# Performance work log

Measured on AMD Instinct MI355X. Metric: run time of the kernel, lower is better.

The kernel has to match this reference:

```python
import jax, jax.numpy as jnp
import numpy as np

E, H, F, T, K = 32, 1024, 512, 1024, 8

def setup_inputs() -> dict:
    key = jax.random.key(0)
    k1, k2, k3, k4, k5 = jax.random.split(key, 5)
    return {
        "hidden_states": jax.random.normal(k1, (T, H), dtype=jnp.float32),
        "top_k_index": jax.random.randint(k2, (T, K), 0, E),
        "top_k_weights": jax.random.uniform(k3, (T, K), dtype=jnp.float32),
        "gate_up_proj": jax.random.normal(k4, (E, 2 * F, H), dtype=jnp.float32),
        "down_proj": jax.random.normal(k5, (E, H, F), dtype=jnp.float32),
    }

def reference(hidden_states, top_k_index, top_k_weights, gate_up_proj, down_proj):
    n_experts = gate_up_proj.shape[0]
    T_ = hidden_states.shape[0]
    # Combine routing weights into dense [T, E] map (duplicates accumulate,
    # matching torch's index_add_ semantics).
    w = jnp.zeros((T_, n_experts), dtype=hidden_states.dtype)
    w = w.at[jnp.arange(T_)[:, None], top_k_index].add(top_k_weights)
    ffn = down_proj.shape[-1]

    def step(final, params):
        Wgu, Wd, we = params  # [2F,H], [H,F], [T]
        gu = hidden_states @ Wgu.T            # [T, 2F]
        gate, up = gu[:, :ffn], gu[:, ffn:]
        out = (jax.nn.silu(gate) * up) @ Wd.T  # [T, H]
        return final + we[:, None] * out, None

    final, _ = jax.lax.scan(step, jnp.zeros_like(hidden_states),
                            (gate_up_proj, down_proj, w.T))
    return final
```

## Files before the change

### kernel.cpp

```cpp
#include <hip/hip_runtime.h>
#include <hip/hip_bf16.h>

#define NE     32
#define HD     1024
#define FF     512
#define NT     1024
#define TOPK   8
#define NPAIR  (NT * TOPK)
#define MAXT2  96

typedef __attribute__((ext_vector_type(8))) short  bf16x8;
typedef __attribute__((ext_vector_type(4))) float  f32x4;

__device__ __forceinline__ unsigned short f2bf_rne(float f) {
    unsigned u = __float_as_uint(f);
    u += 0x7FFFu + ((u >> 16) & 1u);
    return (unsigned short)(u >> 16);
}
__device__ __forceinline__ unsigned pk2(float x, float y) {
    __hip_bfloat162 h = __float22bfloat162_rn(float2{x, y});
    union { __hip_bfloat162 h; unsigned u; } c;
    c.h = h;
    return c.u;
}
__device__ __forceinline__ uint4 pk8q(float4 a, float4 b) {
    uint4 r;
    r.x = pk2(a.x, a.y); r.y = pk2(a.z, a.w);
    r.z = pk2(b.x, b.y); r.w = pk2(b.z, b.w);
    return r;
}
__device__ __forceinline__ bf16x8 pk8r(float4 a, float4 b) {
    union { unsigned u[4]; bf16x8 v; } r;
    r.u[0] = pk2(a.x, a.y); r.u[1] = pk2(a.z, a.w);
    r.u[2] = pk2(b.x, b.y); r.u[3] = pk2(b.z, b.w);
    return r.v;
}
__device__ __forceinline__ void gload16(const void* g, void* l) {
    __builtin_amdgcn_global_load_lds(
        (const __attribute__((address_space(1))) unsigned int*)g,
        (__attribute__((address_space(3))) unsigned int*)l, 16, 0, 0);
}
#define MFMA16(a, b, c) __builtin_amdgcn_mfma_f32_16x16x32_bf16(a, b, c, 0, 0, 0)

#define PIPE_SYNC() do {                                   \
    asm volatile("s_waitcnt vmcnt(6)" ::: "memory");       \
    __builtin_amdgcn_s_barrier();                          \
    __builtin_amdgcn_sched_barrier(0);                     \
} while (0)

#define OFF_XG (128u * 1024u)
#define OFF_AB (OFF_XG + 8320u * 2048u)
#define OFF_O  (OFF_AB + 8320u * 1024u)

__global__ __launch_bounds__(1024) void k_route(const int* __restrict__ idx,
                                                const float* __restrict__ tkw,
                                                int* __restrict__ meta) {
    __shared__ int sc[NE], scur[NE], soff[NE + 1];
    __shared__ int ste[MAXT2], stm[MAXT2], snt;
    int tid = threadIdx.x;
    if (tid < NE) { sc[tid] = 0; scur[tid] = 0; }
    __syncthreads();
    int e8[TOPK];
#pragma unroll
    for (int j = 0; j < TOPK; j++) { e8[j] = idx[tid * TOPK + j]; atomicAdd(&sc[e8[j]], 1); }
    __syncthreads();
    if (tid == 0) {
        int off = 0, nt = 0;
        for (int e = 0; e < NE; e++) {
            soff[e] = off;
            for (int s = 0; s < sc[e]; s += 128) { ste[nt] = e; stm[nt] = s; nt++; }
            off += sc[e];
        }
        soff[NE] = off; snt = nt;
    }
    __syncthreads();
    int*   tok_list = meta + 256;
    float* w_list   = (float*)(meta + 8448);
    int*   posmap   = meta + 16640;
#pragma unroll
    for (int j = 0; j < TOPK; j++) {
        int e = e8[j];
        int p = soff[e] + atomicAdd(&scur[e], 1);
        tok_list[p] = tid;
        w_list[p]   = tkw[tid * TOPK + j];
        posmap[tid * TOPK + j] = p;
    }
    if (tid <= NE) meta[1 + tid] = soff[tid];
    if (tid == 0)  meta[0] = snt;
    if (tid < MAXT2) { meta[64 + tid] = (tid < snt) ? ste[tid] : 0;
                       meta[160 + tid] = (tid < snt) ? stm[tid] : 0; }
}

__global__ void k_gather(const float* __restrict__ hs, const int* __restrict__ meta,
                         unsigned short* __restrict__ Xg) {
    int i = blockIdx.x * blockDim.x + threadIdx.x;
    int p = i >> 7, c = (i & 127) << 3;
    int tok = meta[256 + p];
    float4 a = *(const float4*)(hs + (size_t)tok * HD + c);
    float4 b = *(const float4*)(hs + (size_t)tok * HD + c + 4);
    *(uint4*)(Xg + (size_t)p * HD + c) = pk8q(a, b);
}

__global__ __launch_bounds__(256, 2) void k_mm1(
        const unsigned short* __restrict__ Xg, const float* __restrict__ wgu,
        const int* __restrict__ meta, const float* __restrict__ w_list,
        unsigned short* __restrict__ A) {
    int lid = blockIdx.x;
    int wsw = (lid & 7) * 96 + (lid >> 3);
    int bx = wsw >> 3, by = wsw & 7;
    int numt = meta[0];
    if (bx >= numt) return;
    int e   = meta[64 + bx], m0 = meta[160 + bx];
    int seg = meta[1 + e];
    int nrows = meta[2 + e] - seg - m0;
    if (nrows > 128) nrows = 128;
    int c0 = by * 64;

    __shared__ __align__(16) unsigned char Xb0[8192];
    __shared__ __align__(16) unsigned char Xb1[8192];
    __shared__ __align__(16) unsigned char Xb2[8192];
    int tid = threadIdx.x;
    int wave = tid >> 6, lane = tid & 63, lr = lane & 15, lk = lane >> 4;

    unsigned Lp0 = (unsigned)(wave * 2) * 1024u + (unsigned)lane * 16u;
    unsigned Lp1 = Lp0 + 1024u;
    unsigned ldsoff0 = Lp0, ldsoff1 = Lp1;
    const unsigned char* xsrc0 = (const unsigned char*)Xg +
        (size_t)(seg + m0 + (Lp0 >> 6)) * (HD * 2) + ((Lp0 & 63u) ^ (((Lp0 >> 7) & 3u) << 4));
    const unsigned char* xsrc1 = (const unsigned char*)Xg +
        (size_t)(seg + m0 + (Lp1 >> 6)) * (HD * 2) + ((Lp1 & 63u) ^ (((Lp1 >> 7) & 3u) << 4));

    int cp = c0 + wave * 16 + lr;
    const float* gp = wgu + ((size_t)e * 2 * FF + cp) * HD + lk * 8;
    const float* up = gp + (size_t)FF * HD;

    unsigned aoff[8];
#pragma unroll
    for (int mf = 0; mf < 8; mf++) {
        unsigned row = mf * 16 + lr;
        aoff[mf] = row * 64 + (((unsigned)lk * 16) ^ (((row >> 1) & 3u) << 4));
    }

    f32x4 acc[8][2] = {};
    float4 wsA[4], wsB[4];
    const unsigned char* cur = Xb0;
    const unsigned char* nxt = Xb1;
    const unsigned char* fut = Xb2;

    gload16(xsrc0, Xb0 + ldsoff0); gload16(xsrc1, Xb0 + ldsoff1);
    xsrc0 += 64; xsrc1 += 64;
    gload16(xsrc0, Xb1 + ldsoff0); gload16(xsrc1, Xb1 + ldsoff1);
    xsrc0 += 64; xsrc1 += 64;
    wsA[0] = *(const float4*)(gp);     wsA[1] = *(const float4*)(gp + 4);
    wsA[2] = *(const float4*)(up);     wsA[3] = *(const float4*)(up + 4);
    int wk = 32;

    auto step = [&](float4 (&wuse)[4], float4 (&wld)[4], bool doX, bool doW) {
        PIPE_SYNC();
        if (doX) {
            gload16(xsrc0, (void*)(fut + ldsoff0));
            gload16(xsrc1, (void*)(fut + ldsoff1));
            xsrc0 += 64; xsrc1 += 64;
        }
        if (doW) {
            wld[0] = *(const float4*)(gp + wk);     wld[1] = *(const float4*)(gp + wk + 4);
            wld[2] = *(const float4*)(up + wk);     wld[3] = *(const float4*)(up + wk + 4);
            wk += 32;
        }
        bf16x8 bg = pk8r(wuse[0], wuse[1]);
        bf16x8 bu = pk8r(wuse[2], wuse[3]);
#pragma unroll
        for (int mf = 0; mf < 8; mf++) {
            bf16x8 af = *(const bf16x8*)(cur + aoff[mf]);
            acc[mf][0] = MFMA16(af, bg, acc[mf][0]);
            acc[mf][1] = MFMA16(af, bu, acc[mf][1]);
        }
        const unsigned char* t = cur; cur = nxt; nxt = fut; fut = t;
    };

    for (int t2 = 0; t2 < 14; t2++) {
        step(wsA, wsB, true, true);
        step(wsB, wsA, true, true);
    }
    step(wsA, wsB, true,  true);
    step(wsB, wsA, true,  true);
    step(wsA, wsB, false, true);
    step(wsB, wsA, false, false);

#pragma unroll
    for (int mf = 0; mf < 8; mf++)
#pragma unroll
        for (int q = 0; q < 4; q++) {
            int r = mf * 16 + lk * 4 + q;
            if (r < nrows) {
                float w = w_list[seg + m0 + r];
                float g = acc[mf][0][q], u = acc[mf][1][q];
                float act = (g / (1.f + __expf(-g))) * u * w;
                A[(size_t)(seg + m0 + r) * FF + cp] = f2bf_rne(act);
            }
        }
}

__global__ __launch_bounds__(256, 2) void k_mm2(
        const unsigned short* __restrict__ A, const float* __restrict__ wd,
        const int* __restrict__ meta, float* __restrict__ O) {
    int lid = blockIdx.x;
    int wsw = (lid & 7) * 96 + (lid >> 3);
    int bx = wsw >> 3, by = wsw & 7;
    int numt = meta[0];
    if (bx >= numt) return;
    int e   = meta[64 + bx], m0 = meta[160 + bx];
    int seg = meta[1 + e];
    int nrows = meta[2 + e] - seg - m0;
    if (nrows > 128) nrows = 128;
    int n0 = by * 128;

    __shared__ __align__(16) unsigned char Xb0[8192];
    __shared__ __align__(16) unsigned char Xb1[8192];
    __shared__ __align__(16) unsigned char Xb2[8192];
    int tid = threadIdx.x;
    int wave = tid >> 6, lane = tid & 63, lr = lane & 15, lk = lane >> 4;

    unsigned Lp0 = (unsigned)(wave * 2) * 1024u + (unsigned)lane * 16u;
    unsigned Lp1 = Lp0 + 1024u;
    unsigned ldsoff0 = Lp0, ldsoff1 = Lp1;
    const unsigned char* xsrc0 = (const unsigned char*)A +
        (size_t)(seg + m0 + (Lp0 >> 6)) * (FF * 2) + ((Lp0 & 63u) ^ (((Lp0 >> 7) & 3u) << 4));
    const unsigned char* xsrc1 = (const unsigned char*)A +
        (size_t)(seg + m0 + (Lp1 >> 6)) * (FF * 2) + ((Lp1 & 63u) ^ (((Lp1 >> 7) & 3u) << 4));

    int n_a = n0 + wave * 32 + lr;
    int n_b = n_a + 16;
    const float* wpa = wd + ((size_t)e * HD + n_a) * FF + lk * 8;
    const float* wpb = wd + ((size_t)e * HD + n_b) * FF + lk * 8;

    unsigned aoff[8];
#pragma unroll
    for (int mf = 0; mf < 8; mf++) {
        unsigned row = mf * 16 + lr;
        aoff[mf] = row * 64 + (((unsigned)lk * 16) ^ (((row >> 1) & 3u) << 4));
    }

    f32x4 acc[8][2] = {};
    float4 wsA[4], wsB[4];
    const unsigned char* cur = Xb0;
    const unsigned char* nxt = Xb1;
    const unsigned char* fut = Xb2;

    gload16(xsrc0, Xb0 + ldsoff0); gload16(xsrc1, Xb0 + ldsoff1);
    xsrc0 += 64; xsrc1 += 64;
    gload16(xsrc0, Xb1 + ldsoff0); gload16(xsrc1, Xb1 + ldsoff1);
    xsrc0 += 64; xsrc1 += 64;
    wsA[0] = *(const float4*)(wpa);    wsA[1] = *(const float4*)(wpa + 4);
    wsA[2] = *(const float4*)(wpb);    wsA[3] = *(const float4*)(wpb + 4);
    int wk = 32;

    auto step = [&](float4 (&wuse)[4], float4 (&wld)[4], bool doX, bool doW) {
        PIPE_SYNC();
        if (doX) {
            gload16(xsrc0, (void*)(fut + ldsoff0));
            gload16(xsrc1, (void*)(fut + ldsoff1));
            xsrc0 += 64; xsrc1 += 64;
        }
        if (doW) {
            wld[0] = *(const float4*)(wpa + wk);   wld[1] = *(const float4*)(wpa + wk + 4);
            wld[2] = *(const float4*)(wpb + wk);   wld[3] = *(const float4*)(wpb + wk + 4);
            wk += 32;
        }
        bf16x8 b0 = pk8r(wuse[0], wuse[1]);
        bf16x8 b1 = pk8r(wuse[2], wuse[3]);
#pragma unroll
        for (int mf = 0; mf < 8; mf++) {
            bf16x8 af = *(const bf16x8*)(cur + aoff[mf]);
            acc[mf][0] = MFMA16(af, b0, acc[mf][0]);
            acc[mf][1] = MFMA16(af, b1, acc[mf][1]);
        }
        const unsigned char* t = cur; cur = nxt; nxt = fut; fut = t;
    };

    for (int t2 = 0; t2 < 6; t2++) {
        step(wsA, wsB, true, true);
        step(wsB, wsA, true, true);
    }
    step(wsA, wsB, true,  true);
    step(wsB, wsA, true,  true);
    step(wsA, wsB, false, true);
    step(wsB, wsA, false, false);

#pragma unroll
    for (int mf = 0; mf < 8; mf++)
#pragma unroll
        for (int q = 0; q < 4; q++) {
            int r = mf * 16 + lk * 4 + q;
            if (r < nrows) {
                O[(size_t)(seg + m0 + r) * HD + n_a] = acc[mf][0][q];
                O[(size_t)(seg + m0 + r) * HD + n_b] = acc[mf][1][q];
            }
        }
}

__global__ void k_reduce(const float* __restrict__ O, const int* __restrict__ posmap,
                         float* __restrict__ out) {
    int i = blockIdx.x * blockDim.x + threadIdx.x;
    int t = i >> 8, c4 = i & 255;
    float4 acc = make_float4(0.f, 0.f, 0.f, 0.f);
#pragma unroll
    for (int k = 0; k < TOPK; k++) {
        int p = posmap[t * TOPK + k];
        float4 v = ((const float4*)(O + (size_t)p * HD))[c4];
        acc.x += v.x; acc.y += v.y; acc.z += v.z; acc.w += v.w;
    }
    ((float4*)out)[i] = acc;
}

extern "C" void kernel_launch(void* const* d_in, const int* in_sizes, int n_in,
                              void* d_out, int out_size, void* d_ws, size_t ws_size,
                              hipStream_t stream) {
    const float* hs  = (const float*)d_in[0];
    const int*   idx = (const int*)  d_in[1];
    const float* tkw = (const float*)d_in[2];
    const float* wgu = (const float*)d_in[3];
    const float* wd  = (const float*)d_in[4];
    float* out = (float*)d_out;

    char* ws = (char*)d_ws;
    int* meta = (int*)ws;
    unsigned short* Xg   = (unsigned short*)(ws + OFF_XG);
    unsigned short* A_bf = (unsigned short*)(ws + OFF_AB);
    float* O_rows        = (float*)(ws + OFF_O);
    const float* w_list  = (const float*)(meta + 8448);
    const int* posmap    = meta + 16640;

    k_route<<<1, 1024, 0, stream>>>(idx, tkw, meta);
    k_gather<<<NPAIR * (HD / 8) / 256, 256, 0, stream>>>(hs, meta, Xg);
    k_mm1<<<MAXT2 * 8, 256, 0, stream>>>(Xg, wgu, meta, w_list, A_bf);
    k_mm2<<<MAXT2 * 8, 256, 0, stream>>>(A_bf, wd, meta, O_rows);
    k_reduce<<<NT * HD / 4 / 256, 256, 0, stream>>>(O_rows, posmap, out);
}
```

Measured before the change: 140.6 us.

## Split GEMM tiles across 8 waves and deepen weight-prefetch pipeline

Both expert GEMM kernels now launch 512 threads (8 waves) per block instead of 256. The 128-row tile is split into two 64-row halves across wave pairs, so each wave holds half the accumulators. Each thread issues a single LDS async load per stage. The register weight prefetch gains a third buffer, so global weight loads are issued two steps ahead, with the vmcnt wait adjusted and a full drain on the last step. The aim is more waves in flight to hide global latency and lower register pressure, at the cost of loading each weight fragment twice (once per row-half wave).

```diff
diff --git a/kernel.cpp b/kernel.cpp
--- a/kernel.cpp
+++ b/kernel.cpp
@@ -42,10 +42,11 @@
 }
 #define MFMA16(a, b, c) __builtin_amdgcn_mfma_f32_16x16x32_bf16(a, b, c, 0, 0, 0)
 
-#define PIPE_SYNC() do {                                   \
-    asm volatile("s_waitcnt vmcnt(6)" ::: "memory");       \
-    __builtin_amdgcn_s_barrier();                          \
-    __builtin_amdgcn_sched_barrier(0);                     \
+#define PIPE_SYNC(LAST) do {                                       \
+    if (LAST) asm volatile("s_waitcnt vmcnt(0)" ::: "memory");     \
+    else      asm volatile("s_waitcnt vmcnt(5)" ::: "memory");     \
+    __builtin_amdgcn_s_barrier();                                  \
+    __builtin_amdgcn_sched_barrier(0);                             \
 } while (0)
 
 #define OFF_XG (128u * 1024u)
@@ -101,7 +102,7 @@
     *(uint4*)(Xg + (size_t)p * HD + c) = pk8q(a, b);
 }
 
-__global__ __launch_bounds__(256, 2) void k_mm1(
+__global__ __launch_bounds__(512, 4) void k_mm1(
         const unsigned short* __restrict__ Xg, const float* __restrict__ wgu,
         const int* __restrict__ meta, const float* __restrict__ w_list,
         unsigned short* __restrict__ A) {
@@ -121,48 +122,43 @@
     __shared__ __align__(16) unsigned char Xb2[8192];
     int tid = threadIdx.x;
     int wave = tid >> 6, lane = tid & 63, lr = lane & 15, lk = lane >> 4;
-
-    unsigned Lp0 = (unsigned)(wave * 2) * 1024u + (unsigned)lane * 16u;
-    unsigned Lp1 = Lp0 + 1024u;
-    unsigned ldsoff0 = Lp0, ldsoff1 = Lp1;
-    const unsigned char* xsrc0 = (const unsigned char*)Xg +
-        (size_t)(seg + m0 + (Lp0 >> 6)) * (HD * 2) + ((Lp0 & 63u) ^ (((Lp0 >> 7) & 3u) << 4));
-    const unsigned char* xsrc1 = (const unsigned char*)Xg +
-        (size_t)(seg + m0 + (Lp1 >> 6)) * (HD * 2) + ((Lp1 & 63u) ^ (((Lp1 >> 7) & 3u) << 4));
-
-    int cp = c0 + wave * 16 + lr;
+    int wave_m = wave >> 2, wave_n = wave & 3;
+
+    unsigned Lp = (unsigned)wave * 1024u + (unsigned)lane * 16u;
+    unsigned ldsoff = Lp;
+    const unsigned char* xsrc = (const unsigned char*)Xg +
+        (size_t)(seg + m0 + (Lp >> 6)) * (HD * 2) + ((Lp & 63u) ^ (((Lp >> 7) & 3u) << 4));
+
+    int cp = c0 + wave_n * 16 + lr;
     const float* gp = wgu + ((size_t)e * 2 * FF + cp) * HD + lk * 8;
     const float* up = gp + (size_t)FF * HD;
 
-    unsigned aoff[8];
-#pragma unroll
-    for (int mf = 0; mf < 8; mf++) {
-        unsigned row = mf * 16 + lr;
+    unsigned aoff[4];
+#pragma unroll
+    for (int mf = 0; mf < 4; mf++) {
+        unsigned row = wave_m * 64 + mf * 16 + lr;
         aoff[mf] = row * 64 + (((unsigned)lk * 16) ^ (((row >> 1) & 3u) << 4));
     }
 
-    f32x4 acc[8][2] = {};
-    float4 wsA[4], wsB[4];
+    f32x4 acc[4][2] = {};
+    float4 wsA[4], wsB[4], wsC[4];
     const unsigned char* cur = Xb0;
     const unsigned char* nxt = Xb1;
     const unsigned char* fut = Xb2;
 
-    gload16(xsrc0, Xb0 + ldsoff0); gload16(xsrc1, Xb0 + ldsoff1);
-    xsrc0 += 64; xsrc1 += 64;
-    gload16(xsrc0, Xb1 + ldsoff0); gload16(xsrc1, Xb1 + ldsoff1);
-    xsrc0 += 64; xsrc1 += 64;
-    wsA[0] = *(const float4*)(gp);     wsA[1] = *(const float4*)(gp + 4);
-    wsA[2] = *(const float4*)(up);     wsA[3] = *(const float4*)(up + 4);
-    int wk = 32;
-
-    auto step = [&](float4 (&wuse)[4], float4 (&wld)[4], bool doX, bool doW) {
-        PIPE_SYNC();
-        if (doX) {
-            gload16(xsrc0, (void*)(fut + ldsoff0));
-            gload16(xsrc1, (void*)(fut + ldsoff1));
-            xsrc0 += 64; xsrc1 += 64;
-        }
-        if (doW) {
+    gload16(xsrc, Xb0 + ldsoff); xsrc += 64;
+    gload16(xsrc, Xb1 + ldsoff); xsrc += 64;
+    __builtin_amdgcn_sched_barrier(0);
+    wsA[0] = *(const float4*)(gp);      wsA[1] = *(const float4*)(gp + 4);
+    wsA[2] = *(const float4*)(up);      wsA[3] = *(const float4*)(up + 4);
+    wsB[0] = *(const float4*)(gp + 32); wsB[1] = *(const float4*)(gp + 36);
+    wsB[2] = *(const float4*)(up + 32); wsB[3] = *(const float4*)(up + 36);
+    int wk = 64;
+
+    auto step = [&](float4 (&wuse)[4], float4 (&wld)[4], bool iss, bool last) {
+        PIPE_SYNC(last);
+        if (iss) {
+            gload16(xsrc, (void*)(fut + ldsoff)); xsrc += 64;
             wld[0] = *(const float4*)(gp + wk);     wld[1] = *(const float4*)(gp + wk + 4);
             wld[2] = *(const float4*)(up + wk);     wld[3] = *(const float4*)(up + wk + 4);
             wk += 32;
@@ -170,7 +166,7 @@
         bf16x8 bg = pk8r(wuse[0], wuse[1]);
         bf16x8 bu = pk8r(wuse[2], wuse[3]);
 #pragma unroll
-        for (int mf = 0; mf < 8; mf++) {
+        for (int mf = 0; mf < 4; mf++) {
             bf16x8 af = *(const bf16x8*)(cur + aoff[mf]);
             acc[mf][0] = MFMA16(af, bg, acc[mf][0]);
             acc[mf][1] = MFMA16(af, bu, acc[mf][1]);
@@ -178,20 +174,19 @@
         const unsigned char* t = cur; cur = nxt; nxt = fut; fut = t;
     };
 
-    for (int t2 = 0; t2 < 14; t2++) {
-        step(wsA, wsB, true, true);
-        step(wsB, wsA, true, true);
-    }
-    step(wsA, wsB, true,  true);
-    step(wsB, wsA, true,  true);
-    step(wsA, wsB, false, true);
-    step(wsB, wsA, false, false);
-
-#pragma unroll
-    for (int mf = 0; mf < 8; mf++)
+    for (int i = 0; i < 10; i++) {
+        step(wsA, wsC, true, false);
+        step(wsB, wsA, true, false);
+        step(wsC, wsB, true, false);
+    }
+    step(wsA, wsC, false, false);
+    step(wsB, wsA, false, true);
+
+#pragma unroll
+    for (int mf = 0; mf < 4; mf++)
 #pragma unroll
         for (int q = 0; q < 4; q++) {
-            int r = mf * 16 + lk * 4 + q;
+            int r = wave_m * 64 + mf * 16 + lk * 4 + q;
             if (r < nrows) {
                 float w = w_list[seg + m0 + r];
                 float g = acc[mf][0][q], u = acc[mf][1][q];
@@ -201,7 +196,7 @@
         }
 }
 
-__global__ __launch_bounds__(256, 2) void k_mm2(
+__global__ __launch_bounds__(512, 4) void k_mm2(
         const unsigned short* __restrict__ A, const float* __restrict__ wd,
         const int* __restrict__ meta, float* __restrict__ O) {
     int lid = blockIdx.x;
@@ -220,49 +215,44 @@
     __shared__ __align__(16) unsigned char Xb2[8192];
     int tid = threadIdx.x;
     int wave = tid >> 6, lane = tid & 63, lr = lane & 15, lk = lane >> 4;
-
-    unsigned Lp0 = (unsigned)(wave * 2) * 1024u + (unsigned)lane * 16u;
-    unsigned Lp1 = Lp0 + 1024u;
-    unsigned ldsoff0 = Lp0, ldsoff1 = Lp1;
-    const unsigned char* xsrc0 = (const unsigned char*)A +
-        (size_t)(seg + m0 + (Lp0 >> 6)) * (FF * 2) + ((Lp0 & 63u) ^ (((Lp0 >> 7) & 3u) << 4));
-    const unsigned char* xsrc1 = (const unsigned char*)A +
-        (size_t)(seg + m0 + (Lp1 >> 6)) * (FF * 2) + ((Lp1 & 63u) ^ (((Lp1 >> 7) & 3u) << 4));
-
-    int n_a = n0 + wave * 32 + lr;
+    int wave_m = wave >> 2, wave_n = wave & 3;
+
+    unsigned Lp = (unsigned)wave * 1024u + (unsigned)lane * 16u;
+    unsigned ldsoff = Lp;
+    const unsigned char* xsrc = (const unsigned char*)A +
+        (size_t)(seg + m0 + (Lp >> 6)) * (FF * 2) + ((Lp & 63u) ^ (((Lp >> 7) & 3u) << 4));
+
+    int n_a = n0 + wave_n * 32 + lr;
     int n_b = n_a + 16;
     const float* wpa = wd + ((size_t)e * HD + n_a) * FF + lk * 8;
     const float* wpb = wd + ((size_t)e * HD + n_b) * FF + lk * 8;
 
-    unsigned aoff[8];
-#pragma unroll
-    for (int mf = 0; mf < 8; mf++) {
-        unsigned row = mf * 16 + lr;
+    unsigned aoff[4];
+#pragma unroll
+    for (int mf = 0; mf < 4; mf++) {
+        unsigned row = wave_m * 64 + mf * 16 + lr;
         aoff[mf] = row * 64 + (((unsigned)lk * 16) ^ (((row >> 1) & 3u) << 4));
     }
 
-    f32x4 acc[8][2] = {};
-    float4 wsA[4], wsB[4];
+    f32x4 acc[4][2] = {};
+    float4 wsA[4], wsB[4], wsC[4];
     const unsigned char* cur = Xb0;
     const unsigned char* nxt = Xb1;
     const unsigned char* fut = Xb2;
 
-    gload16(xsrc0, Xb0 + ldsoff0); gload16(xsrc1, Xb0 + ldsoff1);
-    xsrc0 += 64; xsrc1 += 64;
-    gload16(xsrc0, Xb1 + ldsoff0); gload16(xsrc1, Xb1 + ldsoff1);
-    xsrc0 += 64; xsrc1 += 64;
-    wsA[0] = *(const float4*)(wpa);    wsA[1] = *(const float4*)(wpa + 4);
-    wsA[2] = *(const float4*)(wpb);    wsA[3] = *(const float4*)(wpb + 4);
-    int wk = 32;
-
-    auto step = [&](float4 (&wuse)[4], float4 (&wld)[4], bool doX, bool doW) {
-        PIPE_SYNC();
-        if (doX) {
-            gload16(xsrc0, (void*)(fut + ldsoff0));
-            gload16(xsrc1, (void*)(fut + ldsoff1));
-            xsrc0 += 64; xsrc1 += 64;
-        }
-        if (doW) {
+    gload16(xsrc, Xb0 + ldsoff); xsrc += 64;
+    gload16(xsrc, Xb1 + ldsoff); xsrc += 64;
+    __builtin_amdgcn_sched_barrier(0);
+    wsA[0] = *(const float4*)(wpa);      wsA[1] = *(const float4*)(wpa + 4);
+    wsA[2] = *(const float4*)(wpb);      wsA[3] = *(const float4*)(wpb + 4);
+    wsB[0] = *(const float4*)(wpa + 32); wsB[1] = *(const float4*)(wpa + 36);
+    wsB[2] = *(const float4*)(wpb + 32); wsB[3] = *(const float4*)(wpb + 36);
+    int wk = 64;
+
+    auto step = [&](float4 (&wuse)[4], float4 (&wld)[4], bool iss, bool last) {
+        PIPE_SYNC(last);
+        if (iss) {
+            gload16(xsrc, (void*)(fut + ldsoff)); xsrc += 64;
             wld[0] = *(const float4*)(wpa + wk);   wld[1] = *(const float4*)(wpa + wk + 4);
             wld[2] = *(const float4*)(wpb + wk);   wld[3] = *(const float4*)(wpb + wk + 4);
             wk += 32;
@@ -270,7 +260,7 @@
         bf16x8 b0 = pk8r(wuse[0], wuse[1]);
         bf16x8 b1 = pk8r(wuse[2], wuse[3]);
 #pragma unroll
-        for (int mf = 0; mf < 8; mf++) {
+        for (int mf = 0; mf < 4; mf++) {
             bf16x8 af = *(const bf16x8*)(cur + aoff[mf]);
             acc[mf][0] = MFMA16(af, b0, acc[mf][0]);
             acc[mf][1] = MFMA16(af, b1, acc[mf][1]);
@@ -278,20 +268,21 @@
         const unsigned char* t = cur; cur = nxt; nxt = fut; fut = t;
     };
 
-    for (int t2 = 0; t2 < 6; t2++) {
-        step(wsA, wsB, true, true);
-        step(wsB, wsA, true, true);
-    }
-    step(wsA, wsB, true,  true);
-    step(wsB, wsA, true,  true);
-    step(wsA, wsB, false, true);
-    step(wsB, wsA, false, false);
-
-#pragma unroll
-    for (int mf = 0; mf < 8; mf++)
+    for (int i = 0; i < 4; i++) {
+        step(wsA, wsC, true, false);
+        step(wsB, wsA, true, false);
+        step(wsC, wsB, true, false);
+    }
+    step(wsA, wsC, true,  false);
+    step(wsB, wsA, true,  false);
+    step(wsC, wsB, false, false);
+    step(wsA, wsC, false, true);
+
+#pragma unroll
+    for (int mf = 0; mf < 4; mf++)
 #pragma unroll
         for (int q = 0; q < 4; q++) {
-            int r = mf * 16 + lk * 4 + q;
+            int r = wave_m * 64 + mf * 16 + lk * 4 + q;
             if (r < nrows) {
                 O[(size_t)(seg + m0 + r) * HD + n_a] = acc[mf][0][q];
                 O[(size_t)(seg + m0 + r) * HD + n_b] = acc[mf][1][q];
@@ -333,7 +324,7 @@
 
     k_route<<<1, 1024, 0, stream>>>(idx, tkw, meta);
     k_gather<<<NPAIR * (HD / 8) / 256, 256, 0, stream>>>(hs, meta, Xg);
-    k_mm1<<<MAXT2 * 8, 256, 0, stream>>>(Xg, wgu, meta, w_list, A_bf);
-    k_mm2<<<MAXT2 * 8, 256, 0, stream>>>(A_bf, wd, meta, O_rows);
+    k_mm1<<<MAXT2 * 8, 512, 0, stream>>>(Xg, wgu, meta, w_list, A_bf);
+    k_mm2<<<MAXT2 * 8, 512, 0, stream>>>(A_bf, wd, meta, O_rows);
     k_reduce<<<NT * HD / 4 / 256, 256, 0, stream>>>(O_rows, posmap, out);
 }
```

Measured after the change: 197.9 us. 1.41x slower.

## Split MoE GEMM tiles into 2x2 wave layout with half-width N tiles

Applied to the files above, without the earlier changes.

Both grouped GEMM kernels now use a narrower N tile (32 columns for mm1, 64 for mm2) and arrange the four waves as a 2x2 grid over M and N instead of four waves across N. This doubles the number of blocks to fill more CUs, halves per-wave accumulators so occupancy can rise to 4 blocks per CU, and adds a full vmcnt(0) wait before the last step. The cost is that each X tile in LDS is reloaded by twice as many blocks, and each weight column is read by two waves.

```diff
diff --git a/kernel.cpp b/kernel.cpp
--- a/kernel.cpp
+++ b/kernel.cpp
@@ -42,10 +42,11 @@
 }
 #define MFMA16(a, b, c) __builtin_amdgcn_mfma_f32_16x16x32_bf16(a, b, c, 0, 0, 0)
 
-#define PIPE_SYNC() do {                                   \
-    asm volatile("s_waitcnt vmcnt(6)" ::: "memory");       \
-    __builtin_amdgcn_s_barrier();                          \
-    __builtin_amdgcn_sched_barrier(0);                     \
+#define PIPE_SYNC(LAST) do {                                       \
+    if (LAST) asm volatile("s_waitcnt vmcnt(0)" ::: "memory");     \
+    else      asm volatile("s_waitcnt vmcnt(6)" ::: "memory");     \
+    __builtin_amdgcn_s_barrier();                                  \
+    __builtin_amdgcn_sched_barrier(0);                             \
 } while (0)
 
 #define OFF_XG (128u * 1024u)
@@ -101,26 +102,27 @@
     *(uint4*)(Xg + (size_t)p * HD + c) = pk8q(a, b);
 }
 
-__global__ __launch_bounds__(256, 2) void k_mm1(
+__global__ __launch_bounds__(256, 4) void k_mm1(
         const unsigned short* __restrict__ Xg, const float* __restrict__ wgu,
         const int* __restrict__ meta, const float* __restrict__ w_list,
         unsigned short* __restrict__ A) {
     int lid = blockIdx.x;
-    int wsw = (lid & 7) * 96 + (lid >> 3);
-    int bx = wsw >> 3, by = wsw & 7;
+    int wsw = (lid & 7) * 192 + (lid >> 3);
+    int bx = wsw >> 4, by = wsw & 15;
     int numt = meta[0];
     if (bx >= numt) return;
     int e   = meta[64 + bx], m0 = meta[160 + bx];
     int seg = meta[1 + e];
     int nrows = meta[2 + e] - seg - m0;
     if (nrows > 128) nrows = 128;
-    int c0 = by * 64;
+    int c0 = by * 32;
 
     __shared__ __align__(16) unsigned char Xb0[8192];
     __shared__ __align__(16) unsigned char Xb1[8192];
     __shared__ __align__(16) unsigned char Xb2[8192];
     int tid = threadIdx.x;
     int wave = tid >> 6, lane = tid & 63, lr = lane & 15, lk = lane >> 4;
+    int wave_m = wave >> 1, wave_n = wave & 1;
 
     unsigned Lp0 = (unsigned)(wave * 2) * 1024u + (unsigned)lane * 16u;
     unsigned Lp1 = Lp0 + 1024u;
@@ -130,18 +132,18 @@
     const unsigned char* xsrc1 = (const unsigned char*)Xg +
         (size_t)(seg + m0 + (Lp1 >> 6)) * (HD * 2) + ((Lp1 & 63u) ^ (((Lp1 >> 7) & 3u) << 4));
 
-    int cp = c0 + wave * 16 + lr;
+    int cp = c0 + wave_n * 16 + lr;
     const float* gp = wgu + ((size_t)e * 2 * FF + cp) * HD + lk * 8;
     const float* up = gp + (size_t)FF * HD;
 
-    unsigned aoff[8];
-#pragma unroll
-    for (int mf = 0; mf < 8; mf++) {
-        unsigned row = mf * 16 + lr;
+    unsigned aoff[4];
+#pragma unroll
+    for (int mf = 0; mf < 4; mf++) {
+        unsigned row = wave_m * 64 + mf * 16 + lr;
         aoff[mf] = row * 64 + (((unsigned)lk * 16) ^ (((row >> 1) & 3u) << 4));
     }
 
-    f32x4 acc[8][2] = {};
+    f32x4 acc[4][2] = {};
     float4 wsA[4], wsB[4];
     const unsigned char* cur = Xb0;
     const unsigned char* nxt = Xb1;
@@ -155,8 +157,8 @@
     wsA[2] = *(const float4*)(up);     wsA[3] = *(const float4*)(up + 4);
     int wk = 32;
 
-    auto step = [&](float4 (&wuse)[4], float4 (&wld)[4], bool doX, bool doW) {
-        PIPE_SYNC();
+    auto step = [&](float4 (&wuse)[4], float4 (&wld)[4], bool doX, bool doW, bool last) {
+        PIPE_SYNC(last);
         if (doX) {
             gload16(xsrc0, (void*)(fut + ldsoff0));
             gload16(xsrc1, (void*)(fut + ldsoff1));
@@ -170,7 +172,7 @@
         bf16x8 bg = pk8r(wuse[0], wuse[1]);
         bf16x8 bu = pk8r(wuse[2], wuse[3]);
 #pragma unroll
-        for (int mf = 0; mf < 8; mf++) {
+        for (int mf = 0; mf < 4; mf++) {
             bf16x8 af = *(const bf16x8*)(cur + aoff[mf]);
             acc[mf][0] = MFMA16(af, bg, acc[mf][0]);
             acc[mf][1] = MFMA16(af, bu, acc[mf][1]);
@@ -179,19 +181,19 @@
     };
 
     for (int t2 = 0; t2 < 14; t2++) {
-        step(wsA, wsB, true, true);
-        step(wsB, wsA, true, true);
-    }
-    step(wsA, wsB, true,  true);
-    step(wsB, wsA, true,  true);
-    step(wsA, wsB, false, true);
-    step(wsB, wsA, false, false);
-
-#pragma unroll
-    for (int mf = 0; mf < 8; mf++)
+        step(wsA, wsB, true, true, false);
+        step(wsB, wsA, true, true, false);
+    }
+    step(wsA, wsB, true,  true,  false);
+    step(wsB, wsA, true,  true,  false);
+    step(wsA, wsB, false, true,  false);
+    step(wsB, wsA, false, false, true);
+
+#pragma unroll
+    for (int mf = 0; mf < 4; mf++)
 #pragma unroll
         for (int q = 0; q < 4; q++) {
-            int r = mf * 16 + lk * 4 + q;
+            int r = wave_m * 64 + mf * 16 + lk * 4 + q;
             if (r < nrows) {
                 float w = w_list[seg + m0 + r];
                 float g = acc[mf][0][q], u = acc[mf][1][q];
@@ -201,25 +203,26 @@
         }
 }
 
-__global__ __launch_bounds__(256, 2) void k_mm2(
+__global__ __launch_bounds__(256, 4) void k_mm2(
         const unsigned short* __restrict__ A, const float* __restrict__ wd,
         const int* __restrict__ meta, float* __restrict__ O) {
     int lid = blockIdx.x;
-    int wsw = (lid & 7) * 96 + (lid >> 3);
-    int bx = wsw >> 3, by = wsw & 7;
+    int wsw = (lid & 7) * 192 + (lid >> 3);
+    int bx = wsw >> 4, by = wsw & 15;
     int numt = meta[0];
     if (bx >= numt) return;
     int e   = meta[64 + bx], m0 = meta[160 + bx];
     int seg = meta[1 + e];
     int nrows = meta[2 + e] - seg - m0;
     if (nrows > 128) nrows = 128;
-    int n0 = by * 128;
+    int n0 = by * 64;
 
     __shared__ __align__(16) unsigned char Xb0[8192];
     __shared__ __align__(16) unsigned char Xb1[8192];
     __shared__ __align__(16) unsigned char Xb2[8192];
     int tid = threadIdx.x;
     int wave = tid >> 6, lane = tid & 63, lr = lane & 15, lk = lane >> 4;
+    int wave_m = wave >> 1, wave_n = wave & 1;
 
     unsigned Lp0 = (unsigned)(wave * 2) * 1024u + (unsigned)lane * 16u;
     unsigned Lp1 = Lp0 + 1024u;
@@ -229,19 +232,19 @@
     const unsigned char* xsrc1 = (const unsigned char*)A +
         (size_t)(seg + m0 + (Lp1 >> 6)) * (FF * 2) + ((Lp1 & 63u) ^ (((Lp1 >> 7) & 3u) << 4));
 
-    int n_a = n0 + wave * 32 + lr;
+    int n_a = n0 + wave_n * 32 + lr;
     int n_b = n_a + 16;
     const float* wpa = wd + ((size_t)e * HD + n_a) * FF + lk * 8;
     const float* wpb = wd + ((size_t)e * HD + n_b) * FF + lk * 8;
 
-    unsigned aoff[8];
-#pragma unroll
-    for (int mf = 0; mf < 8; mf++) {
-        unsigned row = mf * 16 + lr;
+    unsigned aoff[4];
+#pragma unroll
+    for (int mf = 0; mf < 4; mf++) {
+        unsigned row = wave_m * 64 + mf * 16 + lr;
         aoff[mf] = row * 64 + (((unsigned)lk * 16) ^ (((row >> 1) & 3u) << 4));
     }
 
-    f32x4 acc[8][2] = {};
+    f32x4 acc[4][2] = {};
     float4 wsA[4], wsB[4];
     const unsigned char* cur = Xb0;
     const unsigned char* nxt = Xb1;
@@ -255,8 +258,8 @@
     wsA[2] = *(const float4*)(wpb);    wsA[3] = *(const float4*)(wpb + 4);
     int wk = 32;
 
-    auto step = [&](float4 (&wuse)[4], float4 (&wld)[4], bool doX, bool doW) {
-        PIPE_SYNC();
+    auto step = [&](float4 (&wuse)[4], float4 (&wld)[4], bool doX, bool doW, bool last) {
+        PIPE_SYNC(last);
         if (doX) {
             gload16(xsrc0, (void*)(fut + ldsoff0));
             gload16(xsrc1, (void*)(fut + ldsoff1));
@@ -270,7 +273,7 @@
         bf16x8 b0 = pk8r(wuse[0], wuse[1]);
         bf16x8 b1 = pk8r(wuse[2], wuse[3]);
 #pragma unroll
-        for (int mf = 0; mf < 8; mf++) {
+        for (int mf = 0; mf < 4; mf++) {
             bf16x8 af = *(const bf16x8*)(cur + aoff[mf]);
             acc[mf][0] = MFMA16(af, b0, acc[mf][0]);
             acc[mf][1] = MFMA16(af, b1, acc[mf][1]);
@@ -279,19 +282,19 @@
     };
 
     for (int t2 = 0; t2 < 6; t2++) {
-        step(wsA, wsB, true, true);
-        step(wsB, wsA, true, true);
-    }
-    step(wsA, wsB, true,  true);
-    step(wsB, wsA, true,  true);
-    step(wsA, wsB, false, true);
-    step(wsB, wsA, false, false);
-
-#pragma unroll
-    for (int mf = 0; mf < 8; mf++)
+        step(wsA, wsB, true, true, false);
+        step(wsB, wsA, true, true, false);
+    }
+    step(wsA, wsB, true,  true,  false);
+    step(wsB, wsA, true,  true,  false);
+    step(wsA, wsB, false, true,  false);
+    step(wsB, wsA, false, false, true);
+
+#pragma unroll
+    for (int mf = 0; mf < 4; mf++)
 #pragma unroll
         for (int q = 0; q < 4; q++) {
-            int r = mf * 16 + lk * 4 + q;
+            int r = wave_m * 64 + mf * 16 + lk * 4 + q;
             if (r < nrows) {
                 O[(size_t)(seg + m0 + r) * HD + n_a] = acc[mf][0][q];
                 O[(size_t)(seg + m0 + r) * HD + n_b] = acc[mf][1][q];
@@ -333,7 +336,7 @@
 
     k_route<<<1, 1024, 0, stream>>>(idx, tkw, meta);
     k_gather<<<NPAIR * (HD / 8) / 256, 256, 0, stream>>>(hs, meta, Xg);
-    k_mm1<<<MAXT2 * 8, 256, 0, stream>>>(Xg, wgu, meta, w_list, A_bf);
-    k_mm2<<<MAXT2 * 8, 256, 0, stream>>>(A_bf, wd, meta, O_rows);
+    k_mm1<<<MAXT2 * 16, 256, 0, stream>>>(Xg, wgu, meta, w_list, A_bf);
+    k_mm2<<<MAXT2 * 16, 256, 0, stream>>>(A_bf, wd, meta, O_rows);
     k_reduce<<<NT * HD / 4 / 256, 256, 0, stream>>>(O_rows, posmap, out);
 }
```

New measurement: 222.5 us. 1.58x slower.
